# Kernel tuning notes

Hardware: AMD Instinct MI355X
Metric: run time of the kernel (lower is better)

Reference implementation:

```python
import jax, jax.numpy as jnp
import numpy as np

N_NODES = 100000
N_EDGES = 1600000
IN_DIM, HID_DIM, OUT_DIM = 128, 128, 64


def setup_inputs() -> dict:
    key = jax.random.key(0)
    k1, k2, k3, k4 = jax.random.split(key, 4)
    x = jax.random.normal(k1, (N_NODES, IN_DIM), dtype=jnp.float32)
    edge_index = jax.random.randint(k2, (2, N_EDGES), 0, N_NODES, dtype=jnp.int64)
    W1 = jax.random.normal(k3, (IN_DIM, HID_DIM), dtype=jnp.float32) * (1.0 / np.sqrt(IN_DIM))
    b1 = jnp.zeros((HID_DIM,), dtype=jnp.float32)
    W2 = jax.random.normal(k4, (HID_DIM, OUT_DIM), dtype=jnp.float32) * (1.0 / np.sqrt(HID_DIM))
    b2 = jnp.zeros((OUT_DIM,), dtype=jnp.float32)
    return {"x": x, "edge_index": edge_index, "W1": W1, "b1": b1, "W2": W2, "b2": b2}


def _gcn_conv(h, src, dst, norm, W, b, n_nodes):
    # Dense transform first (PyG GCNConv order), then gather-scatter aggregation.
    h = h @ W                                   # [N, out]
    msg = h[src] * norm[:, None]                # [E, out] gather + scale
    out = jax.ops.segment_sum(msg, dst, num_segments=n_nodes)  # scatter-add
    return out + b


def reference(x, edge_index, W1, b1, W2, b2):
    src, dst = edge_index[0], edge_index[1]
    n = x.shape[0]
    # symmetric normalization: deg from in-degree (unit edge weights), no self loops
    deg = jax.ops.segment_sum(jnp.ones_like(src, dtype=x.dtype), dst, num_segments=n)
    deg_inv_sqrt = jnp.where(deg > 0, jax.lax.rsqrt(jnp.maximum(deg, 1.0)), 0.0)
    norm = deg_inv_sqrt[src] * deg_inv_sqrt[dst]  # [E]
    h = jax.nn.relu(_gcn_conv(x, src, dst, norm, W1, b1, n))
    # dropout is identity in eval mode
    out = _gcn_conv(h, src, dst, norm, W2, b2, n)
    return out
```

## Files before the change

### kernel.cpp

```cpp
#include <hip/hip_runtime.h>
#include <stdint.h>

#define NN 100000
#define NE 1600000
#define K_DIM 128

#define BSH 7
#define NBKT ((NN + (1 << BSH) - 1) >> BSH)
#define EPT 32
#define BIN_CHUNK (256 * EPT)
#define CAP 4096

typedef unsigned int uint32;
typedef unsigned short ushort16;
typedef __attribute__((ext_vector_type(8))) short bf16x8;
typedef __attribute__((ext_vector_type(4))) float f32x4;

__device__ __forceinline__ ushort16 f2bf(float f) {
    uint32 u = __float_as_uint(f);
    u += 0x7fffu + ((u >> 16) & 1u);
    return (ushort16)(u >> 16);
}
__device__ __forceinline__ float bf_lo(uint32 u) { return __uint_as_float(u << 16); }
__device__ __forceinline__ float bf_hi(uint32 u) { return __uint_as_float(u & 0xffff0000u); }

__device__ __forceinline__ void acc8(float* acc, uint4 v) {
    acc[0] += bf_lo(v.x); acc[1] += bf_hi(v.x);
    acc[2] += bf_lo(v.y); acc[3] += bf_hi(v.y);
    acc[4] += bf_lo(v.z); acc[5] += bf_hi(v.z);
    acc[6] += bf_lo(v.w); acc[7] += bf_hi(v.w);
}

__device__ __forceinline__ bf16x8 ld_frag8(const ushort16* p) {
    uint2 lo = *(const uint2*)p;
    uint2 hi = *(const uint2*)(p + 4);
    union { uint32 u[4]; bf16x8 v; } x;
    x.u[0] = lo.x; x.u[1] = lo.y; x.u[2] = hi.x; x.u[3] = hi.y;
    return x.v;
}


__global__ __launch_bounds__(256) void bin_pass1_kernel(
        const int* __restrict__ ei, int* __restrict__ gcursor,
        uint2* __restrict__ staging) {
    __shared__ int hist[NBKT];
    __shared__ int base[NBKT];
    int tid = threadIdx.x;
    int e0 = blockIdx.x * BIN_CHUNK;

    for (int i = tid; i < NBKT; i += 256) hist[i] = 0;
    __syncthreads();

    #pragma unroll
    for (int k = 0; k < EPT; k++) {
        int e = e0 + k * 256 + tid;
        if (e < NE) {
            int d = ei[NE + e];
            atomicAdd(&hist[d >> BSH], 1);
        }
    }
    __syncthreads();

    for (int i = tid; i < NBKT; i += 256) {
        int c = hist[i];
        base[i] = c ? atomicAdd(&gcursor[i], c) : 0;
        hist[i] = 0;
    }
    __syncthreads();

    #pragma unroll
    for (int k = 0; k < EPT; k++) {
        int e = e0 + k * 256 + tid;
        if (e < NE) {
            int s = ei[e];
            int d = ei[NE + e];
            int b = d >> BSH;
            int off = atomicAdd(&hist[b], 1);
            staging[(size_t)b * CAP + base[b] + off] = make_uint2((uint32)s, (uint32)d);
        }
    }
}

__global__ __launch_bounds__(256) void csr_build_kernel(
        const uint2* __restrict__ staging, const int* __restrict__ gcursor,
        float* __restrict__ dis, int* __restrict__ row_start, int* __restrict__ row_end,
        int* __restrict__ ssrc) {
    __shared__ int cnt[1 << BSH];
    __shared__ int sb[1 << BSH];
    __shared__ int cur[1 << BSH];
    __shared__ int pend[1 << BSH];
    int b = blockIdx.x;
    int node0 = b << BSH;
    int tid = threadIdx.x;
    int n_edges = gcursor[b];

    if (tid < (1 << BSH)) cnt[tid] = 0;
    __syncthreads();

    for (int i = tid; i < n_edges; i += 256) {
        uint2 p = staging[(size_t)b * CAP + i];
        atomicAdd(&cnt[p.y & ((1 << BSH) - 1)], 1);
    }
    __syncthreads();

    int p = 0;
    if (tid < (1 << BSH)) {
        int node = node0 + tid;
        p = (node < NN) ? ((cnt[tid] + 7) & ~7) : 0;
        sb[tid] = p;
    }
    __syncthreads();
    #pragma unroll
    for (int off = 1; off < (1 << BSH); off <<= 1) {
        int t = (tid >= off && tid < (1 << BSH)) ? sb[tid - off] : 0;
        __syncthreads();
        if (tid < (1 << BSH)) sb[tid] += t;
        __syncthreads();
    }
    if (tid < (1 << BSH)) {
        int rs = b * CAP + sb[tid] - p;
        cur[tid] = rs;
        pend[tid] = rs + p;
        int node = node0 + tid;
        if (node < NN) {
            row_start[node] = rs;
            row_end[node] = rs + p;
            int c = cnt[tid];
            dis[node] = (c > 0) ? rsqrtf((float)c) : 0.0f;
        }
    }
    __syncthreads();

    for (int i = tid; i < n_edges; i += 256) {
        uint2 pr = staging[(size_t)b * CAP + i];
        int off = atomicAdd(&cur[pr.y & ((1 << BSH) - 1)], 1);
        ssrc[off] = (int)pr.x;
    }
    __syncthreads();

    if (tid < (1 << BSH)) {
        int node = node0 + tid;
        if (node < NN) {
            for (int q = cur[tid]; q < pend[tid]; q++) ssrc[q] = NN;
        }
    }
}

template <int N, bool ABF16>
__global__ __launch_bounds__(256) void gemm_mfma_kernel(
        const void* __restrict__ Ap, const float* __restrict__ W,
        const float* __restrict__ dis, ushort16* __restrict__ out, int M) {
    constexpr int BM = 64, K = K_DIM;
    constexpr int LDA = 132;
    constexpr int NT = N / 16;
    constexpr int NLOG = (N == 128) ? 7 : 6;

    __shared__ ushort16 As[BM * LDA];
    __shared__ ushort16 Bt[N * LDA];

    int tid = threadIdx.x;
    int row0 = blockIdx.x * BM;

    if constexpr (!ABF16) {
        const float* A = (const float*)Ap;
        #pragma unroll
        for (int c = 0; c < 8; c++) {
            int idx = c * 1024 + tid * 4;
            int r = idx >> 7, col = idx & 127;
            int ra = row0 + r;
            float4 v = (ra < M) ? *(const float4*)&A[(size_t)ra * K + col]
                                : make_float4(0.f, 0.f, 0.f, 0.f);
            ushort4 bq;
            bq.x = f2bf(v.x); bq.y = f2bf(v.y); bq.z = f2bf(v.z); bq.w = f2bf(v.w);
            *(ushort4*)&As[r * LDA + col] = bq;
        }
    } else {
        const ushort16* A = (const ushort16*)Ap;
        #pragma unroll
        for (int c = 0; c < 4; c++) {
            int idx = c * 2048 + tid * 8;
            int r = idx >> 7, col = idx & 127;
            int ra = row0 + r;
            uint4 v = make_uint4(0u, 0u, 0u, 0u);
            if (ra < M) v = *(const uint4*)&A[(size_t)ra * K + col];
            *(uint2*)&As[r * LDA + col]     = make_uint2(v.x, v.y);
            *(uint2*)&As[r * LDA + col + 4] = make_uint2(v.z, v.w);
        }
    }
    {
        #pragma unroll
        for (int c = 0; c < (K * N) / 1024; c++) {
            int idx = c * 1024 + tid * 4;
            int k = idx >> NLOG, n = idx & (N - 1);
            float4 v = *(const float4*)&W[idx];
            Bt[(n + 0) * LDA + k] = f2bf(v.x);
            Bt[(n + 1) * LDA + k] = f2bf(v.y);
            Bt[(n + 2) * LDA + k] = f2bf(v.z);
            Bt[(n + 3) * LDA + k] = f2bf(v.w);
        }
    }
    __syncthreads();

    int lane = tid & 63;
    int wv = tid >> 6;
    int m0 = wv * 16;
    int ml = lane & 15;
    int quad = lane >> 4;

    f32x4 acc[NT];
    #pragma unroll
    for (int i = 0; i < NT; i++) acc[i] = (f32x4){0.f, 0.f, 0.f, 0.f};

    #pragma unroll
    for (int ks = 0; ks < 4; ks++) {
        int kof = ks * 32 + quad * 8;
        bf16x8 a = ld_frag8(&As[(m0 + ml) * LDA + kof]);
        #pragma unroll
        for (int nt = 0; nt < NT; nt++) {
            bf16x8 bb = ld_frag8(&Bt[(nt * 16 + ml) * LDA + kof]);
            acc[nt] = __builtin_amdgcn_mfma_f32_16x16x32_bf16(a, bb, acc[nt], 0, 0, 0);
        }
    }

    #pragma unroll
    for (int r = 0; r < 4; r++) {
        int row = row0 + m0 + quad * 4 + r;
        if (row < M) {
            float s = dis[row];
            #pragma unroll
            for (int nt = 0; nt < NT; nt++)
                out[(size_t)row * N + nt * 16 + ml] = f2bf(acc[nt][r] * s);
        }
    }
}

__global__ __launch_bounds__(256) void agg128_kernel(
        const ushort16* __restrict__ g, const int* __restrict__ row_start,
        const int* __restrict__ row_end, const int* __restrict__ ssrc,
        const float* __restrict__ dis, const float* __restrict__ bias,
        ushort16* __restrict__ out) {
    int wave = (blockIdx.x * 256 + threadIdx.x) >> 6;
    int lane = threadIdx.x & 63;
    if (wave >= NN) return;

    int f = lane & 15;
    int gq = lane >> 4;

    int beg = row_start[wave];
    int end = row_end[wave];
    float sc = dis[wave];

    float acc[8] = {};
    for (int e = beg; e < end; e += 8) {
        int idx = ssrc[e + (lane & 7)];
        #pragma unroll
        for (int j = 0; j < 2; j++) {
            int s = __shfl(idx, gq * 2 + j);
            uint4 v = *(const uint4*)&g[(size_t)s * 128 + f * 8];
            acc8(acc, v);
        }
    }
    #pragma unroll
    for (int i = 0; i < 8; i++) {
        acc[i] += __shfl_xor(acc[i], 16);
        acc[i] += __shfl_xor(acc[i], 32);
    }
    if (gq == 0) {
        float4 b0 = *(const float4*)&bias[f * 8];
        float4 b1 = *(const float4*)&bias[f * 8 + 4];
        float o0 = fmaxf(sc * acc[0] + b0.x, 0.f);
        float o1 = fmaxf(sc * acc[1] + b0.y, 0.f);
        float o2 = fmaxf(sc * acc[2] + b0.z, 0.f);
        float o3 = fmaxf(sc * acc[3] + b0.w, 0.f);
        float o4 = fmaxf(sc * acc[4] + b1.x, 0.f);
        float o5 = fmaxf(sc * acc[5] + b1.y, 0.f);
        float o6 = fmaxf(sc * acc[6] + b1.z, 0.f);
        float o7 = fmaxf(sc * acc[7] + b1.w, 0.f);
        uint4 pk;
        pk.x = ((uint32)f2bf(o1) << 16) | (uint32)f2bf(o0);
        pk.y = ((uint32)f2bf(o3) << 16) | (uint32)f2bf(o2);
        pk.z = ((uint32)f2bf(o5) << 16) | (uint32)f2bf(o4);
        pk.w = ((uint32)f2bf(o7) << 16) | (uint32)f2bf(o6);
        *(uint4*)&out[(size_t)wave * 128 + f * 8] = pk;
    }
}

__global__ __launch_bounds__(256) void agg64_kernel(
        const ushort16* __restrict__ g, const int* __restrict__ row_start,
        const int* __restrict__ row_end, const int* __restrict__ ssrc,
        const float* __restrict__ dis, const float* __restrict__ bias,
        float* __restrict__ out) {
    int wave = (blockIdx.x * 256 + threadIdx.x) >> 6;
    int lane = threadIdx.x & 63;
    if (wave >= NN) return;

    int f = lane & 7;
    int gq = lane >> 3;

    int beg = row_start[wave];
    int end = row_end[wave];
    float sc = dis[wave];

    float acc[8] = {};
    for (int e = beg; e < end; e += 8) {
        int idx = ssrc[e + (lane & 7)];
        int s = __shfl(idx, gq);
        uint4 v = *(const uint4*)&g[(size_t)s * 64 + f * 8];
        acc8(acc, v);
    }
    #pragma unroll
    for (int i = 0; i < 8; i++) {
        acc[i] += __shfl_xor(acc[i], 8);
        acc[i] += __shfl_xor(acc[i], 16);
        acc[i] += __shfl_xor(acc[i], 32);
    }
    if (gq == 0) {
        float4 b0 = *(const float4*)&bias[f * 8];
        float4 b1 = *(const float4*)&bias[f * 8 + 4];
        float4 o0, o1;
        o0.x = sc * acc[0] + b0.x; o0.y = sc * acc[1] + b0.y;
        o0.z = sc * acc[2] + b0.z; o0.w = sc * acc[3] + b0.w;
        o1.x = sc * acc[4] + b1.x; o1.y = sc * acc[5] + b1.y;
        o1.z = sc * acc[6] + b1.z; o1.w = sc * acc[7] + b1.w;
        *(float4*)&out[(size_t)wave * 64 + f * 8] = o0;
        *(float4*)&out[(size_t)wave * 64 + f * 8 + 4] = o1;
    }
}

extern "C" void kernel_launch(void* const* d_in, const int* in_sizes, int n_in,
                              void* d_out, int out_size, void* d_ws, size_t ws_size,
                              hipStream_t stream) {
    const float* x  = (const float*)d_in[0];
    const int*   ei = (const int*)d_in[1];
    const float* W1 = (const float*)d_in[2];
    const float* b1 = (const float*)d_in[3];
    const float* W2 = (const float*)d_in[4];
    const float* b2 = (const float*)d_in[5];
    float* out = (float*)d_out;

    char* ws = (char*)d_ws;
    size_t off = 0;
    auto alloc = [&](size_t bytes) {
        void* p = ws + off;
        off = (off + bytes + 255) & ~(size_t)255;
        return p;
    };

    float*    dis        = (float*)alloc(NN * 4);
    int*      row_start  = (int*)alloc(NN * 4);
    int*      row_end    = (int*)alloc(NN * 4);
    int*      gcursor    = (int*)alloc(NBKT * 4);
    int*      ssrc       = (int*)alloc((size_t)NBKT * CAP * 4);
    ushort16* g1         = (ushort16*)alloc((size_t)(NN + 1) * 128 * 2);
    char*     big        = (char*)alloc((size_t)NBKT * CAP * 8);
    uint2*    staging    = (uint2*)big;
    ushort16* h          = (ushort16*)big;
    ushort16* g2         = g1;

    hipMemsetAsync(gcursor, 0, NBKT * 4, stream);
    hipMemsetAsync((char*)g1 + (size_t)NN * 256, 0, 256, stream);

    bin_pass1_kernel<<<(NE + BIN_CHUNK - 1) / BIN_CHUNK, 256, 0, stream>>>(ei, gcursor, staging);
    csr_build_kernel<<<NBKT, 256, 0, stream>>>(staging, gcursor, dis, row_start, row_end, ssrc);

    const int GEMM_BLOCKS = (NN + 63) / 64;
    gemm_mfma_kernel<128, false><<<GEMM_BLOCKS, 256, 0, stream>>>(x, W1, dis, g1, NN);

    const int AGG_BLOCKS = (NN + 3) / 4;
    agg128_kernel<<<AGG_BLOCKS, 256, 0, stream>>>(g1, row_start, row_end, ssrc, dis, b1, h);

    hipMemsetAsync((char*)g2 + (size_t)NN * 128, 0, 128, stream);

    gemm_mfma_kernel<64, true><<<GEMM_BLOCKS, 256, 0, stream>>>(h, W2, dis, g2, NN);

    agg64_kernel<<<AGG_BLOCKS, 256, 0, stream>>>(g2, row_start, row_end, ssrc, dis, b2, out);
}
```

Before: 288.0 us.

## Fuse layer-1 aggregation with layer-2 GEMM and merge memsets into init kernel

The first-layer gather/aggregate is fused with the second-layer dense transform. Each block aggregates 64 nodes into shared memory as bf16, then runs MFMA against W2 directly, so the intermediate h never round-trips through global memory and one launch is removed. The three memsets are replaced by a single init kernel, and the destination indices are cached in registers in the binning pass so they are not reloaded. In exchange, each aggregation block now processes 64 nodes serially per wave, 16 per wave, which may reduce latency hiding and load balance. It also adds shared-memory pressure and extra register use from dcache.

```diff
diff --git a/kernel.cpp b/kernel.cpp
--- a/kernel.cpp
+++ b/kernel.cpp
@@ -39,6 +39,13 @@
     return x.v;
 }
 
+__global__ void init_kernel(int* __restrict__ gcursor, uint32* __restrict__ z1,
+                            uint32* __restrict__ z2) {
+    int tid = threadIdx.x;
+    if (tid < NBKT) gcursor[tid] = 0;
+    if (tid < 64) z1[tid] = 0u;
+    else if (tid < 96) z2[tid - 64] = 0u;
+}
 
 __global__ __launch_bounds__(256) void bin_pass1_kernel(
         const int* __restrict__ ei, int* __restrict__ gcursor,
@@ -47,6 +54,7 @@
     __shared__ int base[NBKT];
     int tid = threadIdx.x;
     int e0 = blockIdx.x * BIN_CHUNK;
+    int dcache[EPT];
 
     for (int i = tid; i < NBKT; i += 256) hist[i] = 0;
     __syncthreads();
@@ -54,10 +62,8 @@
     #pragma unroll
     for (int k = 0; k < EPT; k++) {
         int e = e0 + k * 256 + tid;
-        if (e < NE) {
-            int d = ei[NE + e];
-            atomicAdd(&hist[d >> BSH], 1);
-        }
+        dcache[k] = (e < NE) ? ei[NE + e] : -1;
+        if (dcache[k] >= 0) atomicAdd(&hist[dcache[k] >> BSH], 1);
     }
     __syncthreads();
 
@@ -71,9 +77,9 @@
     #pragma unroll
     for (int k = 0; k < EPT; k++) {
         int e = e0 + k * 256 + tid;
-        if (e < NE) {
+        if (dcache[k] >= 0) {
             int s = ei[e];
-            int d = ei[NE + e];
+            int d = dcache[k];
             int b = d >> BSH;
             int off = atomicAdd(&hist[b], 1);
             staging[(size_t)b * CAP + base[b] + off] = make_uint2((uint32)s, (uint32)d);
@@ -146,14 +152,12 @@
     }
 }
 
-template <int N, bool ABF16>
-__global__ __launch_bounds__(256) void gemm_mfma_kernel(
-        const void* __restrict__ Ap, const float* __restrict__ W,
+__global__ __launch_bounds__(256) void gemm128_kernel(
+        const float* __restrict__ A, const float* __restrict__ W,
         const float* __restrict__ dis, ushort16* __restrict__ out, int M) {
-    constexpr int BM = 64, K = K_DIM;
+    constexpr int BM = 64, K = K_DIM, N = 128;
     constexpr int LDA = 132;
     constexpr int NT = N / 16;
-    constexpr int NLOG = (N == 128) ? 7 : 6;
 
     __shared__ ushort16 As[BM * LDA];
     __shared__ ushort16 Bt[N * LDA];
@@ -161,43 +165,26 @@
     int tid = threadIdx.x;
     int row0 = blockIdx.x * BM;
 
-    if constexpr (!ABF16) {
-        const float* A = (const float*)Ap;
-        #pragma unroll
-        for (int c = 0; c < 8; c++) {
-            int idx = c * 1024 + tid * 4;
-            int r = idx >> 7, col = idx & 127;
-            int ra = row0 + r;
-            float4 v = (ra < M) ? *(const float4*)&A[(size_t)ra * K + col]
-                                : make_float4(0.f, 0.f, 0.f, 0.f);
-            ushort4 bq;
-            bq.x = f2bf(v.x); bq.y = f2bf(v.y); bq.z = f2bf(v.z); bq.w = f2bf(v.w);
-            *(ushort4*)&As[r * LDA + col] = bq;
-        }
-    } else {
-        const ushort16* A = (const ushort16*)Ap;
-        #pragma unroll
-        for (int c = 0; c < 4; c++) {
-            int idx = c * 2048 + tid * 8;
-            int r = idx >> 7, col = idx & 127;
-            int ra = row0 + r;
-            uint4 v = make_uint4(0u, 0u, 0u, 0u);
-            if (ra < M) v = *(const uint4*)&A[(size_t)ra * K + col];
-            *(uint2*)&As[r * LDA + col]     = make_uint2(v.x, v.y);
-            *(uint2*)&As[r * LDA + col + 4] = make_uint2(v.z, v.w);
-        }
-    }
-    {
-        #pragma unroll
-        for (int c = 0; c < (K * N) / 1024; c++) {
-            int idx = c * 1024 + tid * 4;
-            int k = idx >> NLOG, n = idx & (N - 1);
-            float4 v = *(const float4*)&W[idx];
-            Bt[(n + 0) * LDA + k] = f2bf(v.x);
-            Bt[(n + 1) * LDA + k] = f2bf(v.y);
-            Bt[(n + 2) * LDA + k] = f2bf(v.z);
-            Bt[(n + 3) * LDA + k] = f2bf(v.w);
-        }
+    #pragma unroll
+    for (int c = 0; c < 8; c++) {
+        int idx = c * 1024 + tid * 4;
+        int r = idx >> 7, col = idx & 127;
+        int ra = row0 + r;
+        float4 v = (ra < M) ? *(const float4*)&A[(size_t)ra * K + col]
+                            : make_float4(0.f, 0.f, 0.f, 0.f);
+        ushort4 bq;
+        bq.x = f2bf(v.x); bq.y = f2bf(v.y); bq.z = f2bf(v.z); bq.w = f2bf(v.w);
+        *(ushort4*)&As[r * LDA + col] = bq;
+    }
+    #pragma unroll
+    for (int c = 0; c < (K * N) / 1024; c++) {
+        int idx = c * 1024 + tid * 4;
+        int k = idx >> 7, n = idx & (N - 1);
+        float4 v = *(const float4*)&W[idx];
+        Bt[(n + 0) * LDA + k] = f2bf(v.x);
+        Bt[(n + 1) * LDA + k] = f2bf(v.y);
+        Bt[(n + 2) * LDA + k] = f2bf(v.z);
+        Bt[(n + 3) * LDA + k] = f2bf(v.w);
     }
     __syncthreads();
 
@@ -234,54 +221,105 @@
     }
 }
 
-__global__ __launch_bounds__(256) void agg128_kernel(
-        const ushort16* __restrict__ g, const int* __restrict__ row_start,
-        const int* __restrict__ row_end, const int* __restrict__ ssrc,
-        const float* __restrict__ dis, const float* __restrict__ bias,
-        ushort16* __restrict__ out) {
-    int wave = (blockIdx.x * 256 + threadIdx.x) >> 6;
-    int lane = threadIdx.x & 63;
-    if (wave >= NN) return;
+__global__ __launch_bounds__(256) void agg_gemm_kernel(
+        const ushort16* __restrict__ g, const float* __restrict__ W2,
+        const int* __restrict__ row_start, const int* __restrict__ row_end,
+        const int* __restrict__ ssrc, const float* __restrict__ dis,
+        const float* __restrict__ b1, ushort16* __restrict__ g2) {
+    constexpr int LDA = 132;
+    __shared__ ushort16 As[64 * LDA];
+    __shared__ ushort16 Bt[64 * LDA];
+
+    int tid = threadIdx.x;
+    int lane = tid & 63;
+    int wv = tid >> 6;
+    int node0 = blockIdx.x * 64;
+
+    #pragma unroll
+    for (int c = 0; c < 8; c++) {
+        int idx = c * 1024 + tid * 4;
+        int k = idx >> 6, n = idx & 63;
+        float4 v = *(const float4*)&W2[idx];
+        Bt[(n + 0) * LDA + k] = f2bf(v.x);
+        Bt[(n + 1) * LDA + k] = f2bf(v.y);
+        Bt[(n + 2) * LDA + k] = f2bf(v.z);
+        Bt[(n + 3) * LDA + k] = f2bf(v.w);
+    }
 
     int f = lane & 15;
     int gq = lane >> 4;
 
-    int beg = row_start[wave];
-    int end = row_end[wave];
-    float sc = dis[wave];
-
-    float acc[8] = {};
-    for (int e = beg; e < end; e += 8) {
-        int idx = ssrc[e + (lane & 7)];
+    for (int it = 0; it < 16; it++) {
+        int nl = wv * 16 + it;
+        int node = node0 + nl;
+        float acc[8] = {};
+        if (node < NN) {
+            int beg = row_start[node];
+            int end = row_end[node];
+            for (int e = beg; e < end; e += 8) {
+                int idx = ssrc[e + (lane & 7)];
+                #pragma unroll
+                for (int j = 0; j < 2; j++) {
+                    int s = __shfl(idx, gq * 2 + j);
+                    uint4 v = *(const uint4*)&g[(size_t)s * 128 + f * 8];
+                    acc8(acc, v);
+                }
+            }
+        }
         #pragma unroll
-        for (int j = 0; j < 2; j++) {
-            int s = __shfl(idx, gq * 2 + j);
-            uint4 v = *(const uint4*)&g[(size_t)s * 128 + f * 8];
-            acc8(acc, v);
-        }
-    }
-    #pragma unroll
-    for (int i = 0; i < 8; i++) {
-        acc[i] += __shfl_xor(acc[i], 16);
-        acc[i] += __shfl_xor(acc[i], 32);
-    }
-    if (gq == 0) {
-        float4 b0 = *(const float4*)&bias[f * 8];
-        float4 b1 = *(const float4*)&bias[f * 8 + 4];
-        float o0 = fmaxf(sc * acc[0] + b0.x, 0.f);
-        float o1 = fmaxf(sc * acc[1] + b0.y, 0.f);
-        float o2 = fmaxf(sc * acc[2] + b0.z, 0.f);
-        float o3 = fmaxf(sc * acc[3] + b0.w, 0.f);
-        float o4 = fmaxf(sc * acc[4] + b1.x, 0.f);
-        float o5 = fmaxf(sc * acc[5] + b1.y, 0.f);
-        float o6 = fmaxf(sc * acc[6] + b1.z, 0.f);
-        float o7 = fmaxf(sc * acc[7] + b1.w, 0.f);
-        uint4 pk;
-        pk.x = ((uint32)f2bf(o1) << 16) | (uint32)f2bf(o0);
-        pk.y = ((uint32)f2bf(o3) << 16) | (uint32)f2bf(o2);
-        pk.z = ((uint32)f2bf(o5) << 16) | (uint32)f2bf(o4);
-        pk.w = ((uint32)f2bf(o7) << 16) | (uint32)f2bf(o6);
-        *(uint4*)&out[(size_t)wave * 128 + f * 8] = pk;
+        for (int i = 0; i < 8; i++) {
+            acc[i] += __shfl_xor(acc[i], 16);
+            acc[i] += __shfl_xor(acc[i], 32);
+        }
+        if (gq == 0) {
+            float sc = (node < NN) ? dis[node] : 0.f;
+            float4 b0 = *(const float4*)&b1[f * 8];
+            float4 bq = *(const float4*)&b1[f * 8 + 4];
+            float o0 = fmaxf(sc * acc[0] + b0.x, 0.f);
+            float o1 = fmaxf(sc * acc[1] + b0.y, 0.f);
+            float o2 = fmaxf(sc * acc[2] + b0.z, 0.f);
+            float o3 = fmaxf(sc * acc[3] + b0.w, 0.f);
+            float o4 = fmaxf(sc * acc[4] + bq.x, 0.f);
+            float o5 = fmaxf(sc * acc[5] + bq.y, 0.f);
+            float o6 = fmaxf(sc * acc[6] + bq.z, 0.f);
+            float o7 = fmaxf(sc * acc[7] + bq.w, 0.f);
+            uint2 p0, p1;
+            p0.x = ((uint32)f2bf(o1) << 16) | (uint32)f2bf(o0);
+            p0.y = ((uint32)f2bf(o3) << 16) | (uint32)f2bf(o2);
+            p1.x = ((uint32)f2bf(o5) << 16) | (uint32)f2bf(o4);
+            p1.y = ((uint32)f2bf(o7) << 16) | (uint32)f2bf(o6);
+            *(uint2*)&As[nl * LDA + f * 8] = p0;
+            *(uint2*)&As[nl * LDA + f * 8 + 4] = p1;
+        }
+    }
+    __syncthreads();
+
+    int ml = lane & 15;
+    int quad = lane >> 4;
+    f32x4 accd[4];
+    #pragma unroll
+    for (int i = 0; i < 4; i++) accd[i] = (f32x4){0.f, 0.f, 0.f, 0.f};
+
+    #pragma unroll
+    for (int ks = 0; ks < 4; ks++) {
+        int kof = ks * 32 + quad * 8;
+        bf16x8 a = ld_frag8(&As[(wv * 16 + ml) * LDA + kof]);
+        #pragma unroll
+        for (int nt = 0; nt < 4; nt++) {
+            bf16x8 bb = ld_frag8(&Bt[(nt * 16 + ml) * LDA + kof]);
+            accd[nt] = __builtin_amdgcn_mfma_f32_16x16x32_bf16(a, bb, accd[nt], 0, 0, 0);
+        }
+    }
+
+    #pragma unroll
+    for (int r = 0; r < 4; r++) {
+        int row = node0 + wv * 16 + quad * 4 + r;
+        if (row < NN) {
+            float s = dis[row];
+            #pragma unroll
+            for (int nt = 0; nt < 4; nt++)
+                g2[(size_t)row * 64 + nt * 16 + ml] = f2bf(accd[nt][r] * s);
+        }
     }
 }
 
@@ -352,26 +390,20 @@
     int*      gcursor    = (int*)alloc(NBKT * 4);
     int*      ssrc       = (int*)alloc((size_t)NBKT * CAP * 4);
     ushort16* g1         = (ushort16*)alloc((size_t)(NN + 1) * 128 * 2);
-    char*     big        = (char*)alloc((size_t)NBKT * CAP * 8);
-    uint2*    staging    = (uint2*)big;
-    ushort16* h          = (ushort16*)big;
-    ushort16* g2         = g1;
-
-    hipMemsetAsync(gcursor, 0, NBKT * 4, stream);
-    hipMemsetAsync((char*)g1 + (size_t)NN * 256, 0, 256, stream);
+    ushort16* g2         = (ushort16*)alloc((size_t)(NN + 1) * 64 * 2);
+    uint2*    staging    = (uint2*)alloc((size_t)NBKT * CAP * 8);
+
+    init_kernel<<<1, 1024, 0, stream>>>(
+        gcursor, (uint32*)((char*)g1 + (size_t)NN * 256), (uint32*)((char*)g2 + (size_t)NN * 128));
 
     bin_pass1_kernel<<<(NE + BIN_CHUNK - 1) / BIN_CHUNK, 256, 0, stream>>>(ei, gcursor, staging);
     csr_build_kernel<<<NBKT, 256, 0, stream>>>(staging, gcursor, dis, row_start, row_end, ssrc);
 
     const int GEMM_BLOCKS = (NN + 63) / 64;
-    gemm_mfma_kernel<128, false><<<GEMM_BLOCKS, 256, 0, stream>>>(x, W1, dis, g1, NN);
+    gemm128_kernel<<<GEMM_BLOCKS, 256, 0, stream>>>(x, W1, dis, g1, NN);
+
+    agg_gemm_kernel<<<GEMM_BLOCKS, 256, 0, stream>>>(g1, W2, row_start, row_end, ssrc, dis, b1, g2);
 
     const int AGG_BLOCKS = (NN + 3) / 4;
-    agg128_kernel<<<AGG_BLOCKS, 256, 0, stream>>>(g1, row_start, row_end, ssrc, dis, b1, h);
-
-    hipMemsetAsync((char*)g2 + (size_t)NN * 128, 0, 128, stream);
-
-    gemm_mfma_kernel<64, true><<<GEMM_BLOCKS, 256, 0, stream>>>(h, W2, dis, g2, NN);
-
     agg64_kernel<<<AGG_BLOCKS, 256, 0, stream>>>(g2, row_start, row_end, ssrc, dis, b2, out);
 }
```

Measured after the change: 307.0 us. 1.07x slower.
